# Kernel tuning notes

Measured on AMD Instinct MI355X. Metric: run time of the kernel, lower is better.

## Reference

```python
import jax, jax.numpy as jnp
import numpy as np

B, S, H, E = 2, 2048, 16, 64
INV_SCALE = 8.0  # sqrt(head_dim); forward divides scores by this


def setup_inputs() -> dict:
    key = jax.random.key(0)
    ks = jax.random.split(key, 10)
    return {
        "query": jax.random.normal(ks[0], (B, S, H, E), dtype=jnp.float32),
        "key": jax.random.normal(ks[1], (B, S, H, E), dtype=jnp.float32),
        "value": jax.random.normal(ks[2], (B, S, H, E), dtype=jnp.float32),
        "attn_mask": jax.random.randint(ks[3], (B, S), 0, 2, dtype=jnp.int32),
        "Wq": jax.random.normal(ks[4], (E, E), dtype=jnp.float32) / np.sqrt(E),
        "bq": jax.random.normal(ks[5], (E,), dtype=jnp.float32) * 0.02,
        "Wk": jax.random.normal(ks[6], (E, E), dtype=jnp.float32) / np.sqrt(E),
        "bk": jax.random.normal(ks[7], (E,), dtype=jnp.float32) * 0.02,
        "Wv": jax.random.normal(ks[8], (E, E), dtype=jnp.float32) / np.sqrt(E),
        "bv": jax.random.normal(ks[9], (E,), dtype=jnp.float32) * 0.02,
    }


def reference(query, key, value, attn_mask, Wq, bq, Wk, bk, Wv, bv):
    # Linear projections over the last (embed) dim; torch Linear: x @ W.T + b
    q = jnp.einsum('bshe,fe->bhsf', query, Wq) + bq  # [B,H,S,E] (permute 0,2,1,3 fused)
    k = jnp.einsum('bshe,fe->bhsf', key, Wk) + bk
    v = jnp.einsum('bshe,fe->bhsf', value, Wv) + bv
    scores = jnp.einsum('bhqe,bhke->bhqk', q, k) / INV_SCALE  # [B,H,S,S]
    # mask: positions where attn_mask == 0 get -inf, broadcast over (1,1,k_len)
    masked = attn_mask[:, None, None, :] == 0  # [B,1,1,S]
    scores = jnp.where(masked, -jnp.inf, scores)
    attn = jax.nn.softmax(scores, axis=-1)
    out = jnp.einsum('bhqk,bhke->bqhe', attn, v)  # permute back to [B,S,H,E]
    return out
```

## Files before the change

### kernel.cpp

```cpp
#include <hip/hip_runtime.h>


#define BATCH 2
#define SEQ   2048
#define NH    16
#define DE    64
#define LDOF  68
#define NKT   (SEQ / 64)
#define LOG2E 1.44269504088896340736f
#define CSHIFT 16.0f

using bf16x8   = __attribute__((ext_vector_type(8))) __bf16;
using bf16x4   = __attribute__((ext_vector_type(4))) __bf16;
using bf16x2   = __attribute__((ext_vector_type(2))) __bf16;
using floatx2  = __attribute__((ext_vector_type(2))) float;
using floatx4  = __attribute__((ext_vector_type(4))) float;
using floatx16 = __attribute__((ext_vector_type(16))) float;
using ushortx4 = __attribute__((ext_vector_type(4))) unsigned short;
using ushortx8 = __attribute__((ext_vector_type(8))) unsigned short;
using uintx4   = __attribute__((ext_vector_type(4))) unsigned int;
using intx4    = __attribute__((ext_vector_type(4))) int;

__device__ __forceinline__ ushortx4 cvt4(floatx4 f) {
    bf16x4 h = __builtin_convertvector(f, bf16x4);
    return __builtin_bit_cast(ushortx4, h);
}

__device__ __forceinline__ unsigned int pkbf16(float a, float b) {
    floatx2 f = {a, b};
    return __builtin_bit_cast(unsigned int, __builtin_convertvector(f, bf16x2));
}

__device__ __forceinline__ void pl32swap(unsigned int& x, unsigned int& y) {
    __asm__ volatile("v_permlane32_swap_b32 %0, %1" : "+v"(x), "+v"(y));
}

__global__ __launch_bounds__(256) void proj_kernel(
    const float* __restrict__ xq, const float* __restrict__ xk, const float* __restrict__ xv,
    const float* __restrict__ Wq, const float* __restrict__ bq,
    const float* __restrict__ Wk, const float* __restrict__ bk,
    const float* __restrict__ Wv, const float* __restrict__ bv,
    unsigned short* __restrict__ qb, unsigned short* __restrict__ kb,
    unsigned short* __restrict__ vtb)
{
    __shared__ __align__(16) unsigned short Wb[64 * 72];
    __shared__ __align__(16) unsigned short Xb[8 * 1160];
    __shared__ __align__(16) unsigned short Ob[12288];
    __shared__ float blds[64];

    const int t  = threadIdx.x;
    const int bi = blockIdx.x;
    const int hh = bi & 1;
    const int st = (bi >> 1) & 127;
    const int b  = (bi >> 8) & 1;
    const int p  = bi >> 9;
    const int h0 = hh * 8;
    const int lane = t & 63, w = t >> 6, quad = lane >> 4, l16 = lane & 15;

    const float* x    = (p == 0) ? xq : (p == 1) ? xk : xv;
    const float* W    = (p == 0) ? Wq : (p == 1) ? Wk : Wv;
    const float* bias = (p == 0) ? bq : (p == 1) ? bk : bv;

    #pragma unroll
    for (int i = 0; i < 8; ++i) {
        int idx = i * 256 + t;
        int s = idx >> 7, rem = idx & 127, h = rem >> 4, e4 = (rem & 15) * 4;
        floatx4 xv4 = *(const floatx4*)(x + ((size_t)(b * SEQ + st * 16 + s) * NH + h0 + h) * DE + e4);
        *(ushortx4*)&Xb[h * 1160 + s * 72 + e4] = cvt4(xv4);
    }
    #pragma unroll
    for (int i = 0; i < 4; ++i) {
        int idx = i * 256 + t;
        int row = idx >> 4, c4 = (idx & 15) * 4;
        floatx4 wv4 = *(const floatx4*)(W + row * 64 + c4);
        *(ushortx4*)&Wb[row * 72 + c4] = cvt4(wv4);
    }
    if (t < 64) blds[t] = bias[t];
    __syncthreads();

    if (p < 2) {
        bf16x8 a0 = *(const bf16x8*)&Wb[(w * 16 + l16) * 72 + quad * 8];
        bf16x8 a1 = *(const bf16x8*)&Wb[(w * 16 + l16) * 72 + 32 + quad * 8];
        floatx4 bf4 = *(const floatx4*)&blds[w * 16 + quad * 4];
        const float scale = (p == 0) ? 0.125f * LOG2E : 1.0f;
        #pragma unroll
        for (int h = 0; h < 8; ++h) {
            bf16x8 b0 = *(const bf16x8*)&Xb[h * 1160 + l16 * 72 + quad * 8];
            bf16x8 b1 = *(const bf16x8*)&Xb[h * 1160 + l16 * 72 + 32 + quad * 8];
            floatx4 c = {0.f, 0.f, 0.f, 0.f};
            c = __builtin_amdgcn_mfma_f32_16x16x32_bf16(a0, b0, c, 0, 0, 0);
            c = __builtin_amdgcn_mfma_f32_16x16x32_bf16(a1, b1, c, 0, 0, 0);
            floatx4 v;
            v[0] = (c[0] + bf4[0]) * scale; v[1] = (c[1] + bf4[1]) * scale;
            v[2] = (c[2] + bf4[2]) * scale; v[3] = (c[3] + bf4[3]) * scale;
            *(ushortx4*)&Ob[h * 1160 + l16 * 72 + w * 16 + quad * 4] = cvt4(v);
        }
    } else {
        bf16x8 b0 = *(const bf16x8*)&Wb[(w * 16 + l16) * 72 + quad * 8];
        bf16x8 b1 = *(const bf16x8*)&Wb[(w * 16 + l16) * 72 + 32 + quad * 8];
        const float bw = blds[w * 16 + l16];
        #pragma unroll
        for (int h = 0; h < 8; ++h) {
            bf16x8 a0 = *(const bf16x8*)&Xb[h * 1160 + l16 * 72 + quad * 8];
            bf16x8 a1 = *(const bf16x8*)&Xb[h * 1160 + l16 * 72 + 32 + quad * 8];
            floatx4 c = {0.f, 0.f, 0.f, 0.f};
            c = __builtin_amdgcn_mfma_f32_16x16x32_bf16(a0, b0, c, 0, 0, 0);
            c = __builtin_amdgcn_mfma_f32_16x16x32_bf16(a1, b1, c, 0, 0, 0);
            floatx4 v;
            v[0] = c[0] + bw; v[1] = c[1] + bw; v[2] = c[2] + bw; v[3] = c[3] + bw;
            *(ushortx4*)&Ob[h * 1536 + (w * 16 + l16) * 24 + quad * 4] = cvt4(v);
        }
    }
    __syncthreads();

    if (p < 2) {
        unsigned short* dst = (p == 0) ? qb : kb;
        const int rb  = st >> 1;
        const int sl0 = (st & 1) * 16;
        #pragma unroll
        for (int i = 0; i < 4; ++i) {
            int idx = i * 256 + t;
            int j = idx & 7, s = (idx >> 3) & 15, h = idx >> 7;
            ushortx8 v = *(const ushortx8*)&Ob[h * 1160 + s * 72 + j * 8];
            size_t off = ((size_t)((b * 16 + h0 + h) * 64) + rb) * 2048 + j * 256 + (sl0 + s) * 8;
            *(ushortx8*)(dst + off) = v;
        }
    } else {
        const int kt  = st >> 2;
        const int cb  = (st & 3) * 2;
        #pragma unroll
        for (int i = 0; i < 4; ++i) {
            int idx = i * 256 + t;
            int cl = idx & 1, e = (idx >> 1) & 63, h = idx >> 7;
            ushortx8 v = *(const ushortx8*)&Ob[h * 1536 + e * 24 + cl * 8];
            size_t off = (((size_t)(b * 16 + h0 + h) * 32 + kt) * 8 + cb + cl) * 512 + e * 8;
            *(ushortx8*)(vtb + off) = v;
        }
    }
}

__global__ __launch_bounds__(512, 2) void attn_kernel(
    const unsigned short* __restrict__ qb, const unsigned short* __restrict__ kb,
    const unsigned short* __restrict__ vtb, const int* __restrict__ mask,
    float* __restrict__ out)
{
    __shared__ __align__(16) char smem[69632 + 4096 + 8192];
    float* Ol = (float*)smem;
    float* Ll = (float*)(smem + 69632);
    float* Ml = (float*)(smem + 73728);

    const int wg  = blockIdx.x;
    const int bh  = ((wg >> 3) >> 3) * 8 + (wg & 7);
    const int qt  = (wg >> 3) & 7;
    const int b   = bh >> 4, h = bh & 15;
    const int q0  = qt * 256;
    const int t   = threadIdx.x;
    const int lane = t & 63, w = t >> 6;
    const int hi = lane >> 5, l31 = lane & 31;
    const int qw = w & 3, kblk = w >> 2;

    {
        intx4 mv = *(const intx4*)(mask + b * SEQ + t * 4);
        Ml[t * 4 + 0] = mv[0] ? -CSHIFT : -1e30f;
        Ml[t * 4 + 1] = mv[1] ? -CSHIFT : -1e30f;
        Ml[t * 4 + 2] = mv[2] ? -CSHIFT : -1e30f;
        Ml[t * 4 + 3] = mv[3] ? -CSHIFT : -1e30f;
    }

    const unsigned short* qpa = qb + ((size_t)(bh * 64 + qt * 8 + qw * 2)) * 2048 + hi * 256 + l31 * 8;
    const unsigned short* kp  = kb + ((size_t)(bh * 64 + kblk)) * 2048 + hi * 256 + l31 * 8;
    const unsigned short* vp  = vtb + (size_t)bh * 131072 + (kblk * 4 + hi) * 512 + l31 * 8;
    const float* Mb = Ml + kblk * 32 + hi * 4;

    bf16x8 qfa[4], qfb[4];
    #pragma unroll
    for (int ks = 0; ks < 4; ++ks) {
        qfa[ks] = *(const bf16x8*)(qpa + ks * 512);
        qfb[ks] = *(const bf16x8*)(qpa + 2048 + ks * 512);
    }

    __syncthreads();

    floatx16 oa0, oa1, ob0, ob1;
    #pragma unroll
    for (int i = 0; i < 16; ++i) { oa0[i] = 0.f; oa1[i] = 0.f; ob0[i] = 0.f; ob1[i] = 0.f; }
    float lpa = 0.f, lpb = 0.f;

    bf16x8 kf0 = *(const bf16x8*)(kp);
    bf16x8 kf1 = *(const bf16x8*)(kp + 512);
    bf16x8 kf2 = *(const bf16x8*)(kp + 1024);
    bf16x8 kf3 = *(const bf16x8*)(kp + 1536);
    bf16x8 vf00 = *(const bf16x8*)(vp);
    bf16x8 vf01 = *(const bf16x8*)(vp + 256);
    bf16x8 vf10 = *(const bf16x8*)(vp + 1024);
    bf16x8 vf11 = *(const bf16x8*)(vp + 1280);
    floatx4 mb0 = *(const floatx4*)(Mb);
    floatx4 mb1 = *(const floatx4*)(Mb + 8);
    floatx4 mb2 = *(const floatx4*)(Mb + 16);
    floatx4 mb3 = *(const floatx4*)(Mb + 24);

    for (int kt = 0; kt < NKT; ++kt) {
        const int ktn = (kt + 1) & (NKT - 1);

        floatx16 sa, sb;
        #pragma unroll
        for (int j = 0; j < 4; ++j) {
            sa[j]      = mb0[j]; sb[j]      = mb0[j];
            sa[4 + j]  = mb1[j]; sb[4 + j]  = mb1[j];
            sa[8 + j]  = mb2[j]; sb[8 + j]  = mb2[j];
            sa[12 + j] = mb3[j]; sb[12 + j] = mb3[j];
        }
        __builtin_amdgcn_s_setprio(1);
        sa = __builtin_amdgcn_mfma_f32_32x32x16_bf16(kf0, qfa[0], sa, 0, 0, 0);
        sa = __builtin_amdgcn_mfma_f32_32x32x16_bf16(kf1, qfa[1], sa, 0, 0, 0);
        sa = __builtin_amdgcn_mfma_f32_32x32x16_bf16(kf2, qfa[2], sa, 0, 0, 0);
        sa = __builtin_amdgcn_mfma_f32_32x32x16_bf16(kf3, qfa[3], sa, 0, 0, 0);
        sb = __builtin_amdgcn_mfma_f32_32x32x16_bf16(kf0, qfb[0], sb, 0, 0, 0);
        sb = __builtin_amdgcn_mfma_f32_32x32x16_bf16(kf1, qfb[1], sb, 0, 0, 0);
        sb = __builtin_amdgcn_mfma_f32_32x32x16_bf16(kf2, qfb[2], sb, 0, 0, 0);
        sb = __builtin_amdgcn_mfma_f32_32x32x16_bf16(kf3, qfb[3], sb, 0, 0, 0);
        __builtin_amdgcn_s_setprio(0);

        {
            const unsigned short* kq = kp + ktn * 4096;
            kf0 = *(const bf16x8*)(kq);
            kf1 = *(const bf16x8*)(kq + 512);
            kf2 = *(const bf16x8*)(kq + 1024);
            kf3 = *(const bf16x8*)(kq + 1536);
            const float* Mn = Mb + ktn * 64;
            mb0 = *(const floatx4*)(Mn);
            mb1 = *(const floatx4*)(Mn + 8);
            mb2 = *(const floatx4*)(Mn + 16);
            mb3 = *(const floatx4*)(Mn + 24);
        }

        #pragma unroll
        for (int r = 0; r < 16; ++r) sa[r] = __builtin_amdgcn_exp2f(sa[r]);
        #pragma unroll
        for (int r = 0; r < 16; ++r) sb[r] = __builtin_amdgcn_exp2f(sb[r]);
        {
            float a0 = sa[0] + sa[1],   a1 = sa[2] + sa[3];
            float a2 = sa[4] + sa[5],   a3 = sa[6] + sa[7];
            float a4 = sa[8] + sa[9],   a5 = sa[10] + sa[11];
            float a6 = sa[12] + sa[13], a7 = sa[14] + sa[15];
            lpa += ((a0 + a1) + (a2 + a3)) + ((a4 + a5) + (a6 + a7));
            float b0 = sb[0] + sb[1],   b1 = sb[2] + sb[3];
            float b2 = sb[4] + sb[5],   b3 = sb[6] + sb[7];
            float b4 = sb[8] + sb[9],   b5 = sb[10] + sb[11];
            float b6 = sb[12] + sb[13], b7 = sb[14] + sb[15];
            lpb += ((b0 + b1) + (b2 + b3)) + ((b4 + b5) + (b6 + b7));
        }

        unsigned int a_w0 = pkbf16(sa[0], sa[1]),   a_w1 = pkbf16(sa[2], sa[3]);
        unsigned int a_w2 = pkbf16(sa[4], sa[5]),   a_w3 = pkbf16(sa[6], sa[7]);
        unsigned int a_w4 = pkbf16(sa[8], sa[9]),   a_w5 = pkbf16(sa[10], sa[11]);
        unsigned int a_w6 = pkbf16(sa[12], sa[13]), a_w7 = pkbf16(sa[14], sa[15]);
        pl32swap(a_w0, a_w2); pl32swap(a_w1, a_w3);
        pl32swap(a_w4, a_w6); pl32swap(a_w5, a_w7);
        uintx4 fa0 = {a_w0, a_w1, a_w2, a_w3};
        uintx4 fa1 = {a_w4, a_w5, a_w6, a_w7};
        bf16x8 pf0a = __builtin_bit_cast(bf16x8, fa0);
        bf16x8 pf1a = __builtin_bit_cast(bf16x8, fa1);
        unsigned int b_w0 = pkbf16(sb[0], sb[1]),   b_w1 = pkbf16(sb[2], sb[3]);
        unsigned int b_w2 = pkbf16(sb[4], sb[5]),   b_w3 = pkbf16(sb[6], sb[7]);
        unsigned int b_w4 = pkbf16(sb[8], sb[9]),   b_w5 = pkbf16(sb[10], sb[11]);
        unsigned int b_w6 = pkbf16(sb[12], sb[13]), b_w7 = pkbf16(sb[14], sb[15]);
        pl32swap(b_w0, b_w2); pl32swap(b_w1, b_w3);
        pl32swap(b_w4, b_w6); pl32swap(b_w5, b_w7);
        uintx4 fb0 = {b_w0, b_w1, b_w2, b_w3};
        uintx4 fb1 = {b_w4, b_w5, b_w6, b_w7};
        bf16x8 pf0b = __builtin_bit_cast(bf16x8, fb0);
        bf16x8 pf1b = __builtin_bit_cast(bf16x8, fb1);

        __builtin_amdgcn_s_setprio(1);
        oa0 = __builtin_amdgcn_mfma_f32_32x32x16_bf16(vf00, pf0a, oa0, 0, 0, 0);
        oa1 = __builtin_amdgcn_mfma_f32_32x32x16_bf16(vf01, pf0a, oa1, 0, 0, 0);
        oa0 = __builtin_amdgcn_mfma_f32_32x32x16_bf16(vf10, pf1a, oa0, 0, 0, 0);
        oa1 = __builtin_amdgcn_mfma_f32_32x32x16_bf16(vf11, pf1a, oa1, 0, 0, 0);
        ob0 = __builtin_amdgcn_mfma_f32_32x32x16_bf16(vf00, pf0b, ob0, 0, 0, 0);
        ob1 = __builtin_amdgcn_mfma_f32_32x32x16_bf16(vf01, pf0b, ob1, 0, 0, 0);
        ob0 = __builtin_amdgcn_mfma_f32_32x32x16_bf16(vf10, pf1b, ob0, 0, 0, 0);
        ob1 = __builtin_amdgcn_mfma_f32_32x32x16_bf16(vf11, pf1b, ob1, 0, 0, 0);
        __builtin_amdgcn_s_setprio(0);

        {
            const unsigned short* vq = vp + ktn * 4096;
            vf00 = *(const bf16x8*)(vq);
            vf01 = *(const bf16x8*)(vq + 256);
            vf10 = *(const bf16x8*)(vq + 1024);
            vf11 = *(const bf16x8*)(vq + 1280);
        }
    }

    const int qa  = qw * 64 + l31;
    const int qbr = qa + 32;
    Ll[qa * 4 + kblk * 2 + hi]  = lpa;
    Ll[qbr * 4 + kblk * 2 + hi] = lpb;
    if (kblk == 1) {
        #pragma unroll
        for (int g = 0; g < 4; ++g) {
            floatx4 ta0 = {oa0[4*g+0], oa0[4*g+1], oa0[4*g+2], oa0[4*g+3]};
            *(floatx4*)&Ol[qa * LDOF + g * 8 + hi * 4] = ta0;
            floatx4 ta1 = {oa1[4*g+0], oa1[4*g+1], oa1[4*g+2], oa1[4*g+3]};
            *(floatx4*)&Ol[qa * LDOF + 32 + g * 8 + hi * 4] = ta1;
            floatx4 tb0 = {ob0[4*g+0], ob0[4*g+1], ob0[4*g+2], ob0[4*g+3]};
            *(floatx4*)&Ol[qbr * LDOF + g * 8 + hi * 4] = tb0;
            floatx4 tb1 = {ob1[4*g+0], ob1[4*g+1], ob1[4*g+2], ob1[4*g+3]};
            *(floatx4*)&Ol[qbr * LDOF + 32 + g * 8 + hi * 4] = tb1;
        }
    }
    __syncthreads();
    if (kblk == 0) {
        floatx4 lva = *(const floatx4*)&Ll[qa * 4];
        float invla = __builtin_amdgcn_rcpf(lva[0] + lva[1] + lva[2] + lva[3]);
        floatx4 lvb = *(const floatx4*)&Ll[qbr * 4];
        float invlb = __builtin_amdgcn_rcpf(lvb[0] + lvb[1] + lvb[2] + lvb[3]);
        #pragma unroll
        for (int g = 0; g < 4; ++g) {
            floatx4 ta0 = *(floatx4*)&Ol[qa * LDOF + g * 8 + hi * 4];
            ta0[0] = (ta0[0] + oa0[4*g+0]) * invla; ta0[1] = (ta0[1] + oa0[4*g+1]) * invla;
            ta0[2] = (ta0[2] + oa0[4*g+2]) * invla; ta0[3] = (ta0[3] + oa0[4*g+3]) * invla;
            *(floatx4*)&Ol[qa * LDOF + g * 8 + hi * 4] = ta0;
            floatx4 ta1 = *(floatx4*)&Ol[qa * LDOF + 32 + g * 8 + hi * 4];
            ta1[0] = (ta1[0] + oa1[4*g+0]) * invla; ta1[1] = (ta1[1] + oa1[4*g+1]) * invla;
            ta1[2] = (ta1[2] + oa1[4*g+2]) * invla; ta1[3] = (ta1[3] + oa1[4*g+3]) * invla;
            *(floatx4*)&Ol[qa * LDOF + 32 + g * 8 + hi * 4] = ta1;
            floatx4 tb0 = *(floatx4*)&Ol[qbr * LDOF + g * 8 + hi * 4];
            tb0[0] = (tb0[0] + ob0[4*g+0]) * invlb; tb0[1] = (tb0[1] + ob0[4*g+1]) * invlb;
            tb0[2] = (tb0[2] + ob0[4*g+2]) * invlb; tb0[3] = (tb0[3] + ob0[4*g+3]) * invlb;
            *(floatx4*)&Ol[qbr * LDOF + g * 8 + hi * 4] = tb0;
            floatx4 tb1 = *(floatx4*)&Ol[qbr * LDOF + 32 + g * 8 + hi * 4];
            tb1[0] = (tb1[0] + ob1[4*g+0]) * invlb; tb1[1] = (tb1[1] + ob1[4*g+1]) * invlb;
            tb1[2] = (tb1[2] + ob1[4*g+2]) * invlb; tb1[3] = (tb1[3] + ob1[4*g+3]) * invlb;
            *(floatx4*)&Ol[qbr * LDOF + 32 + g * 8 + hi * 4] = tb1;
        }
    }
    __syncthreads();
    {
        const int quad = lane >> 4, l16 = lane & 15;
        #pragma unroll
        for (int pass = 0; pass < 8; ++pass) {
            int rl  = w * 32 + pass * 4 + quad;
            int col = l16 * 4;
            floatx4 tv = *(const floatx4*)&Ol[rl * LDOF + col];
            *(floatx4*)(out + (((size_t)b * SEQ + q0 + rl) * NH + h) * DE + col) = tv;
        }
    }
}

extern "C" void kernel_launch(void* const* d_in, const int* in_sizes, int n_in,
                              void* d_out, int out_size, void* d_ws, size_t ws_size,
                              hipStream_t stream) {
    const float* query = (const float*)d_in[0];
    const float* key   = (const float*)d_in[1];
    const float* value = (const float*)d_in[2];
    const int*   mask  = (const int*)d_in[3];
    const float* Wq = (const float*)d_in[4];
    const float* bq = (const float*)d_in[5];
    const float* Wk = (const float*)d_in[6];
    const float* bk = (const float*)d_in[7];
    const float* Wv = (const float*)d_in[8];
    const float* bv = (const float*)d_in[9];

    const size_t tensor_elems = (size_t)BATCH * NH * SEQ * DE;
    unsigned short* qb  = (unsigned short*)d_ws;
    unsigned short* kb  = qb + tensor_elems;
    unsigned short* vtb = kb + tensor_elems;

    proj_kernel<<<dim3(3 * BATCH * 128 * 2), 256, 0, stream>>>(
        query, key, value, Wq, bq, Wk, bk, Wv, bv, qb, kb, vtb);
    attn_kernel<<<dim3(256), 512, 0, stream>>>(
        qb, kb, vtb, mask, (float*)d_out);
}
```

Measured before the change: 146.6 us.

## Stage K/V tiles through LDS with triple-buffered async global_load_lds pipeline

```diff
diff --git a/kernel.cpp b/kernel.cpp
--- a/kernel.cpp
+++ b/kernel.cpp
@@ -33,6 +33,12 @@
 
 __device__ __forceinline__ void pl32swap(unsigned int& x, unsigned int& y) {
     __asm__ volatile("v_permlane32_swap_b32 %0, %1" : "+v"(x), "+v"(y));
+}
+
+__device__ __forceinline__ void glds16(const unsigned short* g, unsigned short* l) {
+    __builtin_amdgcn_global_load_lds(
+        (const __attribute__((address_space(1))) unsigned int*)g,
+        (__attribute__((address_space(3))) unsigned int*)l, 16, 0, 0);
 }
 
 __global__ __launch_bounds__(256) void proj_kernel(
@@ -144,10 +150,11 @@
     const unsigned short* __restrict__ vtb, const int* __restrict__ mask,
     float* __restrict__ out)
 {
-    __shared__ __align__(16) char smem[69632 + 4096 + 8192];
+    __shared__ __align__(16) char smem[73728];
+    unsigned short* KV = (unsigned short*)smem;
+    float* Ml = (float*)(smem + 49152);
     float* Ol = (float*)smem;
     float* Ll = (float*)(smem + 69632);
-    float* Ml = (float*)(smem + 73728);
 
     const int wg  = blockIdx.x;
     const int bh  = ((wg >> 3) >> 3) * 8 + (wg & 7);
@@ -159,6 +166,19 @@
     const int hi = lane >> 5, l31 = lane & 31;
     const int qw = w & 3, kblk = w >> 2;
 
+    const unsigned short* kT = kb + (size_t)(bh * 64) * 2048;
+    const unsigned short* vT = vtb + (size_t)bh * 131072;
+
+    glds16(kT + w * 512 + lane * 8, KV + w * 512);
+    glds16(vT + w * 512 + lane * 8, KV + 4096 + w * 512);
+
+    const unsigned short* qpa = qb + ((size_t)(bh * 64 + qt * 8 + qw * 2)) * 2048 + hi * 256 + l31 * 8;
+    bf16x8 qfa[4], qfb[4];
+    #pragma unroll
+    for (int ks = 0; ks < 4; ++ks) {
+        qfa[ks] = *(const bf16x8*)(qpa + ks * 512);
+        qfb[ks] = *(const bf16x8*)(qpa + 2048 + ks * 512);
+    }
     {
         intx4 mv = *(const intx4*)(mask + b * SEQ + t * 4);
         Ml[t * 4 + 0] = mv[0] ? -CSHIFT : -1e30f;
@@ -166,109 +186,113 @@
         Ml[t * 4 + 2] = mv[2] ? -CSHIFT : -1e30f;
         Ml[t * 4 + 3] = mv[3] ? -CSHIFT : -1e30f;
     }
-
-    const unsigned short* qpa = qb + ((size_t)(bh * 64 + qt * 8 + qw * 2)) * 2048 + hi * 256 + l31 * 8;
-    const unsigned short* kp  = kb + ((size_t)(bh * 64 + kblk)) * 2048 + hi * 256 + l31 * 8;
-    const unsigned short* vp  = vtb + (size_t)bh * 131072 + (kblk * 4 + hi) * 512 + l31 * 8;
-    const float* Mb = Ml + kblk * 32 + hi * 4;
-
-    bf16x8 qfa[4], qfb[4];
-    #pragma unroll
-    for (int ks = 0; ks < 4; ++ks) {
-        qfa[ks] = *(const bf16x8*)(qpa + ks * 512);
-        qfb[ks] = *(const bf16x8*)(qpa + 2048 + ks * 512);
-    }
-
-    __syncthreads();
+    glds16(kT + 4096 + w * 512 + lane * 8, KV + 8192 + w * 512);
+    glds16(vT + 4096 + w * 512 + lane * 8, KV + 8192 + 4096 + w * 512);
+
+    __asm__ volatile("s_waitcnt lgkmcnt(0)" ::: "memory");
+    __builtin_amdgcn_s_barrier();
+
+    const float* Mlb = Ml + kblk * 32 + hi * 4;
 
     floatx16 oa0, oa1, ob0, ob1;
     #pragma unroll
     for (int i = 0; i < 16; ++i) { oa0[i] = 0.f; oa1[i] = 0.f; ob0[i] = 0.f; ob1[i] = 0.f; }
     float lpa = 0.f, lpb = 0.f;
 
-    bf16x8 kf0 = *(const bf16x8*)(kp);
-    bf16x8 kf1 = *(const bf16x8*)(kp + 512);
-    bf16x8 kf2 = *(const bf16x8*)(kp + 1024);
-    bf16x8 kf3 = *(const bf16x8*)(kp + 1536);
-    bf16x8 vf00 = *(const bf16x8*)(vp);
-    bf16x8 vf01 = *(const bf16x8*)(vp + 256);
-    bf16x8 vf10 = *(const bf16x8*)(vp + 1024);
-    bf16x8 vf11 = *(const bf16x8*)(vp + 1280);
-    floatx4 mb0 = *(const floatx4*)(Mb);
-    floatx4 mb1 = *(const floatx4*)(Mb + 8);
-    floatx4 mb2 = *(const floatx4*)(Mb + 16);
-    floatx4 mb3 = *(const floatx4*)(Mb + 24);
+    int coff = 0;
+    int soff = 16384;
 
     for (int kt = 0; kt < NKT; ++kt) {
-        const int ktn = (kt + 1) & (NKT - 1);
-
-        floatx16 sa, sb;
+        if (kt == NKT - 1) { __asm__ volatile("s_waitcnt vmcnt(0)" ::: "memory"); }
+        else               { __asm__ volatile("s_waitcnt vmcnt(2)" ::: "memory"); }
+        __builtin_amdgcn_s_barrier();
+
+        if (kt + 2 < NKT) {
+            const unsigned short* ks2 = kT + (size_t)(kt + 2) * 4096;
+            const unsigned short* vs2 = vT + (size_t)(kt + 2) * 4096;
+            glds16(ks2 + w * 512 + lane * 8, KV + soff + w * 512);
+            glds16(vs2 + w * 512 + lane * 8, KV + soff + 4096 + w * 512);
+        }
+
+        const unsigned short* Kc = KV + coff + kblk * 2048 + hi * 256 + l31 * 8;
+        const unsigned short* Vc = KV + coff + 4096 + (kblk * 4 + hi) * 512 + l31 * 8;
+        const float* Mc = Mlb + kt * 64;
+
+        floatx4 m0 = *(const floatx4*)(Mc);
+        floatx4 m1 = *(const floatx4*)(Mc + 8);
+        floatx4 m2 = *(const floatx4*)(Mc + 16);
+        floatx4 m3 = *(const floatx4*)(Mc + 24);
+
+        bf16x8 kf0 = *(const bf16x8*)(Kc);
+        bf16x8 kf1 = *(const bf16x8*)(Kc + 512);
+        bf16x8 kf2 = *(const bf16x8*)(Kc + 1024);
+        bf16x8 kf3 = *(const bf16x8*)(Kc + 1536);
+
+        floatx16 sa;
         #pragma unroll
         for (int j = 0; j < 4; ++j) {
-            sa[j]      = mb0[j]; sb[j]      = mb0[j];
-            sa[4 + j]  = mb1[j]; sb[4 + j]  = mb1[j];
-            sa[8 + j]  = mb2[j]; sb[8 + j]  = mb2[j];
-            sa[12 + j] = mb3[j]; sb[12 + j] = mb3[j];
+            sa[j] = m0[j]; sa[4 + j] = m1[j]; sa[8 + j] = m2[j]; sa[12 + j] = m3[j];
         }
         __builtin_amdgcn_s_setprio(1);
         sa = __builtin_amdgcn_mfma_f32_32x32x16_bf16(kf0, qfa[0], sa, 0, 0, 0);
         sa = __builtin_amdgcn_mfma_f32_32x32x16_bf16(kf1, qfa[1], sa, 0, 0, 0);
         sa = __builtin_amdgcn_mfma_f32_32x32x16_bf16(kf2, qfa[2], sa, 0, 0, 0);
         sa = __builtin_amdgcn_mfma_f32_32x32x16_bf16(kf3, qfa[3], sa, 0, 0, 0);
-        sb = __builtin_amdgcn_mfma_f32_32x32x16_bf16(kf0, qfb[0], sb, 0, 0, 0);
-        sb = __builtin_amdgcn_mfma_f32_32x32x16_bf16(kf1, qfb[1], sb, 0, 0, 0);
-        sb = __builtin_amdgcn_mfma_f32_32x32x16_bf16(kf2, qfb[2], sb, 0, 0, 0);
-        sb = __builtin_amdgcn_mfma_f32_32x32x16_bf16(kf3, qfb[3], sb, 0, 0, 0);
         __builtin_amdgcn_s_setprio(0);
-
-        {
-            const unsigned short* kq = kp + ktn * 4096;
-            kf0 = *(const bf16x8*)(kq);
-            kf1 = *(const bf16x8*)(kq + 512);
-            kf2 = *(const bf16x8*)(kq + 1024);
-            kf3 = *(const bf16x8*)(kq + 1536);
-            const float* Mn = Mb + ktn * 64;
-            mb0 = *(const floatx4*)(Mn);
-            mb1 = *(const floatx4*)(Mn + 8);
-            mb2 = *(const floatx4*)(Mn + 16);
-            mb3 = *(const floatx4*)(Mn + 24);
-        }
-
         #pragma unroll
         for (int r = 0; r < 16; ++r) sa[r] = __builtin_amdgcn_exp2f(sa[r]);
-        #pragma unroll
-        for (int r = 0; r < 16; ++r) sb[r] = __builtin_amdgcn_exp2f(sb[r]);
         {
             float a0 = sa[0] + sa[1],   a1 = sa[2] + sa[3];
             float a2 = sa[4] + sa[5],   a3 = sa[6] + sa[7];
             float a4 = sa[8] + sa[9],   a5 = sa[10] + sa[11];
             float a6 = sa[12] + sa[13], a7 = sa[14] + sa[15];
             lpa += ((a0 + a1) + (a2 + a3)) + ((a4 + a5) + (a6 + a7));
+        }
+        unsigned int aw0 = pkbf16(sa[0], sa[1]),   aw1 = pkbf16(sa[2], sa[3]);
+        unsigned int aw2 = pkbf16(sa[4], sa[5]),   aw3 = pkbf16(sa[6], sa[7]);
+        unsigned int aw4 = pkbf16(sa[8], sa[9]),   aw5 = pkbf16(sa[10], sa[11]);
+        unsigned int aw6 = pkbf16(sa[12], sa[13]), aw7 = pkbf16(sa[14], sa[15]);
+        pl32swap(aw0, aw2); pl32swap(aw1, aw3);
+        pl32swap(aw4, aw6); pl32swap(aw5, aw7);
+        uintx4 fa0 = {aw0, aw1, aw2, aw3};
+        uintx4 fa1 = {aw4, aw5, aw6, aw7};
+        bf16x8 pf0a = __builtin_bit_cast(bf16x8, fa0);
+        bf16x8 pf1a = __builtin_bit_cast(bf16x8, fa1);
+
+        floatx16 sb;
+        #pragma unroll
+        for (int j = 0; j < 4; ++j) {
+            sb[j] = m0[j]; sb[4 + j] = m1[j]; sb[8 + j] = m2[j]; sb[12 + j] = m3[j];
+        }
+        __builtin_amdgcn_s_setprio(1);
+        sb = __builtin_amdgcn_mfma_f32_32x32x16_bf16(kf0, qfb[0], sb, 0, 0, 0);
+        sb = __builtin_amdgcn_mfma_f32_32x32x16_bf16(kf1, qfb[1], sb, 0, 0, 0);
+        sb = __builtin_amdgcn_mfma_f32_32x32x16_bf16(kf2, qfb[2], sb, 0, 0, 0);
+        sb = __builtin_amdgcn_mfma_f32_32x32x16_bf16(kf3, qfb[3], sb, 0, 0, 0);
+        __builtin_amdgcn_s_setprio(0);
+
+        bf16x8 vf00 = *(const bf16x8*)(Vc);
+        bf16x8 vf01 = *(const bf16x8*)(Vc + 256);
+        bf16x8 vf10 = *(const bf16x8*)(Vc + 1024);
+        bf16x8 vf11 = *(const bf16x8*)(Vc + 1280);
+
+        #pragma unroll
+        for (int r = 0; r < 16; ++r) sb[r] = __builtin_amdgcn_exp2f(sb[r]);
+        {
             float b0 = sb[0] + sb[1],   b1 = sb[2] + sb[3];
             float b2 = sb[4] + sb[5],   b3 = sb[6] + sb[7];
             float b4 = sb[8] + sb[9],   b5 = sb[10] + sb[11];
             float b6 = sb[12] + sb[13], b7 = sb[14] + sb[15];
             lpb += ((b0 + b1) + (b2 + b3)) + ((b4 + b5) + (b6 + b7));
         }
-
-        unsigned int a_w0 = pkbf16(sa[0], sa[1]),   a_w1 = pkbf16(sa[2], sa[3]);
-        unsigned int a_w2 = pkbf16(sa[4], sa[5]),   a_w3 = pkbf16(sa[6], sa[7]);
-        unsigned int a_w4 = pkbf16(sa[8], sa[9]),   a_w5 = pkbf16(sa[10], sa[11]);
-        unsigned int a_w6 = pkbf16(sa[12], sa[13]), a_w7 = pkbf16(sa[14], sa[15]);
-        pl32swap(a_w0, a_w2); pl32swap(a_w1, a_w3);
-        pl32swap(a_w4, a_w6); pl32swap(a_w5, a_w7);
-        uintx4 fa0 = {a_w0, a_w1, a_w2, a_w3};
-        uintx4 fa1 = {a_w4, a_w5, a_w6, a_w7};
-        bf16x8 pf0a = __builtin_bit_cast(bf16x8, fa0);
-        bf16x8 pf1a = __builtin_bit_cast(bf16x8, fa1);
-        unsigned int b_w0 = pkbf16(sb[0], sb[1]),   b_w1 = pkbf16(sb[2], sb[3]);
-        unsigned int b_w2 = pkbf16(sb[4], sb[5]),   b_w3 = pkbf16(sb[6], sb[7]);
-        unsigned int b_w4 = pkbf16(sb[8], sb[9]),   b_w5 = pkbf16(sb[10], sb[11]);
-        unsigned int b_w6 = pkbf16(sb[12], sb[13]), b_w7 = pkbf16(sb[14], sb[15]);
-        pl32swap(b_w0, b_w2); pl32swap(b_w1, b_w3);
-        pl32swap(b_w4, b_w6); pl32swap(b_w5, b_w7);
-        uintx4 fb0 = {b_w0, b_w1, b_w2, b_w3};
-        uintx4 fb1 = {b_w4, b_w5, b_w6, b_w7};
+        unsigned int bw0 = pkbf16(sb[0], sb[1]),   bw1 = pkbf16(sb[2], sb[3]);
+        unsigned int bw2 = pkbf16(sb[4], sb[5]),   bw3 = pkbf16(sb[6], sb[7]);
+        unsigned int bw4 = pkbf16(sb[8], sb[9]),   bw5 = pkbf16(sb[10], sb[11]);
+        unsigned int bw6 = pkbf16(sb[12], sb[13]), bw7 = pkbf16(sb[14], sb[15]);
+        pl32swap(bw0, bw2); pl32swap(bw1, bw3);
+        pl32swap(bw4, bw6); pl32swap(bw5, bw7);
+        uintx4 fb0 = {bw0, bw1, bw2, bw3};
+        uintx4 fb1 = {bw4, bw5, bw6, bw7};
         bf16x8 pf0b = __builtin_bit_cast(bf16x8, fb0);
         bf16x8 pf1b = __builtin_bit_cast(bf16x8, fb1);
 
@@ -283,19 +307,15 @@
         ob1 = __builtin_amdgcn_mfma_f32_32x32x16_bf16(vf11, pf1b, ob1, 0, 0, 0);
         __builtin_amdgcn_s_setprio(0);
 
-        {
-            const unsigned short* vq = vp + ktn * 4096;
-            vf00 = *(const bf16x8*)(vq);
-            vf01 = *(const bf16x8*)(vq + 256);
-            vf10 = *(const bf16x8*)(vq + 1024);
-            vf11 = *(const bf16x8*)(vq + 1280);
-        }
+        coff = (coff == 16384) ? 0 : coff + 8192;
+        soff = (soff == 16384) ? 0 : soff + 8192;
     }
 
     const int qa  = qw * 64 + l31;
-    const int qbr = qa + 32;
+    const int qrb = qa + 32;
     Ll[qa * 4 + kblk * 2 + hi]  = lpa;
-    Ll[qbr * 4 + kblk * 2 + hi] = lpb;
+    Ll[qrb * 4 + kblk * 2 + hi] = lpb;
+    __syncthreads();
     if (kblk == 1) {
         #pragma unroll
         for (int g = 0; g < 4; ++g) {
@@ -304,16 +324,16 @@
             floatx4 ta1 = {oa1[4*g+0], oa1[4*g+1], oa1[4*g+2], oa1[4*g+3]};
             *(floatx4*)&Ol[qa * LDOF + 32 + g * 8 + hi * 4] = ta1;
             floatx4 tb0 = {ob0[4*g+0], ob0[4*g+1], ob0[4*g+2], ob0[4*g+3]};
-            *(floatx4*)&Ol[qbr * LDOF + g * 8 + hi * 4] = tb0;
+            *(floatx4*)&Ol[qrb * LDOF + g * 8 + hi * 4] = tb0;
             floatx4 tb1 = {ob1[4*g+0], ob1[4*g+1], ob1[4*g+2], ob1[4*g+3]};
-            *(floatx4*)&Ol[qbr * LDOF + 32 + g * 8 + hi * 4] = tb1;
+            *(floatx4*)&Ol[qrb * LDOF + 32 + g * 8 + hi * 4] = tb1;
         }
     }
     __syncthreads();
     if (kblk == 0) {
         floatx4 lva = *(const floatx4*)&Ll[qa * 4];
         float invla = __builtin_amdgcn_rcpf(lva[0] + lva[1] + lva[2] + lva[3]);
-        floatx4 lvb = *(const floatx4*)&Ll[qbr * 4];
+        floatx4 lvb = *(const floatx4*)&Ll[qrb * 4];
         float invlb = __builtin_amdgcn_rcpf(lvb[0] + lvb[1] + lvb[2] + lvb[3]);
         #pragma unroll
         for (int g = 0; g < 4; ++g) {
@@ -325,14 +345,14 @@
             ta1[0] = (ta1[0] + oa1[4*g+0]) * invla; ta1[1] = (ta1[1] + oa1[4*g+1]) * invla;
             ta1[2] = (ta1[2] + oa1[4*g+2]) * invla; ta1[3] = (ta1[3] + oa1[4*g+3]) * invla;
             *(floatx4*)&Ol[qa * LDOF + 32 + g * 8 + hi * 4] = ta1;
-            floatx4 tb0 = *(floatx4*)&Ol[qbr * LDOF + g * 8 + hi * 4];
+            floatx4 tb0 = *(floatx4*)&Ol[qrb * LDOF + g * 8 + hi * 4];
             tb0[0] = (tb0[0] + ob0[4*g+0]) * invlb; tb0[1] = (tb0[1] + ob0[4*g+1]) * invlb;
             tb0[2] = (tb0[2] + ob0[4*g+2]) * invlb; tb0[3] = (tb0[3] + ob0[4*g+3]) * invlb;
-            *(floatx4*)&Ol[qbr * LDOF + g * 8 + hi * 4] = tb0;
-            floatx4 tb1 = *(floatx4*)&Ol[qbr * LDOF + 32 + g * 8 + hi * 4];
+            *(floatx4*)&Ol[qrb * LDOF + g * 8 + hi * 4] = tb0;
+            floatx4 tb1 = *(floatx4*)&Ol[qrb * LDOF + 32 + g * 8 + hi * 4];
             tb1[0] = (tb1[0] + ob1[4*g+0]) * invlb; tb1[1] = (tb1[1] + ob1[4*g+1]) * invlb;
             tb1[2] = (tb1[2] + ob1[4*g+2]) * invlb; tb1[3] = (tb1[3] + ob1[4*g+3]) * invlb;
-            *(floatx4*)&Ol[qbr * LDOF + 32 + g * 8 + hi * 4] = tb1;
+            *(floatx4*)&Ol[qrb * LDOF + 32 + g * 8 + hi * 4] = tb1;
         }
     }
     __syncthreads();
```

After: 149.7 us. 1.02x slower.
